# Kernel tuning notes

Hardware: AMD Instinct MI355X
Metric: run time of the kernel (lower is better)

## Reference

```python
import jax, jax.numpy as jnp
import numpy as np

D_EMBED = 1024
HEAD_SIZE = 64
BATCH = 8
SEQ = 2048


def setup_inputs() -> dict:
    key = jax.random.key(0)
    kx, kq, kk, kv = jax.random.split(key, 4)
    x = jax.random.normal(kx, (BATCH, SEQ, D_EMBED), dtype=jnp.float32)
    Wq = jax.random.normal(kq, (D_EMBED, HEAD_SIZE), dtype=jnp.float32) * (1.0 / np.sqrt(D_EMBED))
    Wk = jax.random.normal(kk, (D_EMBED, HEAD_SIZE), dtype=jnp.float32) * (1.0 / np.sqrt(D_EMBED))
    Wv = jax.random.normal(kv, (D_EMBED, HEAD_SIZE), dtype=jnp.float32) * (1.0 / np.sqrt(D_EMBED))
    return {"x": x, "Wq": Wq, "Wk": Wk, "Wv": Wv}


def reference(x, Wq, Wk, Wv):
    # x: [B, S, D]; projections -> [B, S, H]
    Q = jnp.einsum('bsd,dh->bsh', x, Wq)
    K = jnp.einsum('bsd,dh->bsh', x, Wk)
    V = jnp.einsum('bsd,dh->bsh', x, Wv)
    S = x.shape[1]
    scores = jnp.einsum('bqh,bkh->bqk', Q, K)  # [B, S, S]
    causal = jnp.tril(jnp.ones((S, S), dtype=bool))
    # mask before scaling (scaling -inf is still -inf; matches original order)
    scores = jnp.where(causal, scores, -jnp.inf)
    scores = scores / jnp.sqrt(jnp.asarray(K.shape[-1], dtype=scores.dtype))
    attn = jax.nn.softmax(scores, axis=-1)
    # dropout_rate = 0.0 (eval): identity
    return jnp.einsum('bqk,bkh->bqh', attn, V)
```

## Files before the change

### kernel.cpp

```cpp
#include <hip/hip_runtime.h>

typedef _Float16 half8_t __attribute__((ext_vector_type(8)));
typedef _Float16 half4_t __attribute__((ext_vector_type(4)));
typedef _Float16 half2_t __attribute__((ext_vector_type(2)));
typedef __fp16 fp16x2 __attribute__((ext_vector_type(2)));
typedef float f32x4 __attribute__((ext_vector_type(4)));

static constexpr int SEQ = 2048;
static constexpr int DEMB = 1024;


__device__ __forceinline__ float fexp2(float x) {
#if __has_builtin(__builtin_amdgcn_exp2f)
  return __builtin_amdgcn_exp2f(x);
#else
  return exp2f(x);
#endif
}

__device__ __forceinline__ half8_t cvt8(float4 a, float4 b) {
  half8_t xf;
  xf[0] = (_Float16)a.x; xf[1] = (_Float16)a.y;
  xf[2] = (_Float16)a.z; xf[3] = (_Float16)a.w;
  xf[4] = (_Float16)b.x; xf[5] = (_Float16)b.y;
  xf[6] = (_Float16)b.z; xf[7] = (_Float16)b.w;
  return xf;
}

__global__ __launch_bounds__(256) void wt_kernel(const float* __restrict__ Wq,
                                                 const float* __restrict__ Wk,
                                                 const float* __restrict__ Wv,
                                                 _Float16* __restrict__ Wt) {
  int i = blockIdx.x * 256 + threadIdx.x;
  int n = i >> 10;
  int k = i & 1023;
  const float* W = (n < 64) ? Wq : ((n < 128) ? Wk : Wv);
  Wt[i] = (_Float16)W[k * 64 + (n & 63)];
}

__global__ __launch_bounds__(256) void proj_kernel(const float* __restrict__ x,
                                                   const _Float16* __restrict__ Wt,
                                                   _Float16* __restrict__ Qh,
                                                   _Float16* __restrict__ Kh,
                                                   _Float16* __restrict__ Vt) {
  __shared__ __align__(16) char sbuf[8192];

  const int tid = threadIdx.x;
  const int lane = tid & 63;
  const int wv = tid >> 6;
  const int g = lane >> 4;
  const int c = lane & 15;
  const int m0 = blockIdx.x * 32;

  const int srow = tid >> 3;
  const float* xsrc = x + (size_t)(m0 + srow) * DEMB + (tid & 7) * 4;
  char* lws = sbuf + ((unsigned)(tid * 16) ^ (unsigned)((srow & 7) << 4));

  const unsigned sw = (unsigned)((c & 7) << 4);
  const unsigned rA = (unsigned)(c * 128 + g * 32);

  const f32x4 zero = {0.f, 0.f, 0.f, 0.f};
  f32x4 acc[2][3];
#pragma unroll
  for (int ms = 0; ms < 2; ++ms)
#pragma unroll
    for (int j = 0; j < 3; ++j) acc[ms][j] = zero;

  const _Float16* wb0 = Wt + (size_t)((3 * wv + 0) * 16 + c) * 1024 + 8 * g;
  const _Float16* wb1 = Wt + (size_t)((3 * wv + 1) * 16 + c) * 1024 + 8 * g;
  const _Float16* wb2 = Wt + (size_t)((3 * wv + 2) * 16 + c) * 1024 + 8 * g;
  half8_t wf0 = *(const half8_t*)(wb0);
  half8_t wf1 = *(const half8_t*)(wb1);
  half8_t wf2 = *(const half8_t*)(wb2);

  {
    float4 xa = *(const float4*)(xsrc);
    *(float4*)(lws) = xa;
  }
  __syncthreads();

  for (int t = 0; t < 31; ++t) {
    const int kc = (t + 1) * 32;
    float4 xn = *(const float4*)(xsrc + kc);
    half8_t wn0 = *(const half8_t*)(wb0 + kc);
    half8_t wn1 = *(const half8_t*)(wb1 + kc);
    half8_t wn2 = *(const half8_t*)(wb2 + kc);
    const char* rb = sbuf + (t & 1) * 4096;
    half8_t xf[2];
#pragma unroll
    for (int ms = 0; ms < 2; ++ms) {
      const unsigned base = rA + (unsigned)(ms * 2048);
      float4 xlo = *(const float4*)(rb + (base ^ sw));
      float4 xhi = *(const float4*)(rb + ((base + 16) ^ sw));
      xf[ms] = cvt8(xlo, xhi);
    }
#pragma unroll
    for (int j = 0; j < 3; ++j) {
      half8_t wcur = (j == 0) ? wf0 : ((j == 1) ? wf1 : wf2);
      const int nt = 3 * wv + j;
      if (nt < 8) {
        acc[0][j] = __builtin_amdgcn_mfma_f32_16x16x32_f16(wcur, xf[0], acc[0][j], 0, 0, 0);
        acc[1][j] = __builtin_amdgcn_mfma_f32_16x16x32_f16(wcur, xf[1], acc[1][j], 0, 0, 0);
      } else {
        acc[0][j] = __builtin_amdgcn_mfma_f32_16x16x32_f16(xf[0], wcur, acc[0][j], 0, 0, 0);
        acc[1][j] = __builtin_amdgcn_mfma_f32_16x16x32_f16(xf[1], wcur, acc[1][j], 0, 0, 0);
      }
    }
    wf0 = wn0; wf1 = wn1; wf2 = wn2;
    *(float4*)(lws + ((t + 1) & 1) * 4096) = xn;
    __syncthreads();
  }
  {
    const char* rb = sbuf + 4096;
    half8_t xf[2];
#pragma unroll
    for (int ms = 0; ms < 2; ++ms) {
      const unsigned base = rA + (unsigned)(ms * 2048);
      float4 xlo = *(const float4*)(rb + (base ^ sw));
      float4 xhi = *(const float4*)(rb + ((base + 16) ^ sw));
      xf[ms] = cvt8(xlo, xhi);
    }
#pragma unroll
    for (int j = 0; j < 3; ++j) {
      half8_t wcur = (j == 0) ? wf0 : ((j == 1) ? wf1 : wf2);
      const int nt = 3 * wv + j;
      if (nt < 8) {
        acc[0][j] = __builtin_amdgcn_mfma_f32_16x16x32_f16(wcur, xf[0], acc[0][j], 0, 0, 0);
        acc[1][j] = __builtin_amdgcn_mfma_f32_16x16x32_f16(wcur, xf[1], acc[1][j], 0, 0, 0);
      } else {
        acc[0][j] = __builtin_amdgcn_mfma_f32_16x16x32_f16(xf[0], wcur, acc[0][j], 0, 0, 0);
        acc[1][j] = __builtin_amdgcn_mfma_f32_16x16x32_f16(xf[1], wcur, acc[1][j], 0, 0, 0);
      }
    }
  }

  const int b = m0 >> 11;
#pragma unroll
  for (int j = 0; j < 3; ++j) {
    const int nt = 3 * wv + j;
#pragma unroll
    for (int ms = 0; ms < 2; ++ms) {
      half4_t h;
      h[0] = (_Float16)acc[ms][j][0]; h[1] = (_Float16)acc[ms][j][1];
      h[2] = (_Float16)acc[ms][j][2]; h[3] = (_Float16)acc[ms][j][3];
      if (nt < 4) {
        *(half4_t*)(Qh + (size_t)(m0 + ms * 16 + c) * 64 + nt * 16 + 4 * g) = h;
      } else if (nt < 8) {
        *(half4_t*)(Kh + (size_t)(m0 + ms * 16 + c) * 64 + (nt - 4) * 16 + 4 * g) = h;
      } else {
        const int hh = (nt - 8) * 16 + c;
        const int s0 = (m0 & 2047) + ms * 16 + 4 * g;
        *(half4_t*)(Vt + (size_t)(b * 64 + hh) * 2048 + s0) = h;
      }
    }
  }
}

__device__ __forceinline__ void flash_tile(int q0, int wv, int g, int c,
                                           const _Float16* __restrict__ Qb,
                                           const _Float16* __restrict__ Kb,
                                           const _Float16* __restrict__ Vb,
                                           f32x4 (&acc)[4], float& m2, float& lsum) {
  const f32x4 zero = {0.f, 0.f, 0.f, 0.f};
  const float CS = 0.18033688011112042f;
  const int q_lane = q0 + c;
  const int nb = ((q0 + 15) >> 6) + 1;

  const _Float16* Qrow = Qb + (size_t)(q0 + c) * 64;
  half8_t qf0 = *(const half8_t*)(Qrow + 8 * g);
  half8_t qf1 = *(const half8_t*)(Qrow + 32 + 8 * g);

  const int addr_u01 = (2 * (g & 1)) * 64 + c * 4;
  const int addr_u23 = (2 * (g & 1) + 1) * 64 + c * 4;
  const bool glo = (g < 2);

  for (int jb = wv; jb < nb; jb += 8) {
    const int k0 = jb * 64;
    f32x4 sacc[4];
#pragma unroll
    for (int kt = 0; kt < 4; ++kt) {
      const _Float16* Krow = Kb + (size_t)(k0 + kt * 16 + c) * 64;
      half8_t kf0 = *(const half8_t*)(Krow + 8 * g);
      half8_t kf1 = *(const half8_t*)(Krow + 32 + 8 * g);
      f32x4 t = zero;
      t = __builtin_amdgcn_mfma_f32_16x16x32_f16(kf0, qf0, t, 0, 0, 0);
      t = __builtin_amdgcn_mfma_f32_16x16x32_f16(kf1, qf1, t, 0, 0, 0);
      sacc[kt] = t;
    }
    half8_t vf0[4], vf1[4];
#pragma unroll
    for (int ht = 0; ht < 4; ++ht) {
      const _Float16* Vrow = Vb + (size_t)(16 * ht + c) * 2048 + k0;
      vf0[ht] = *(const half8_t*)(Vrow + 8 * g);
      vf1[ht] = *(const half8_t*)(Vrow + 32 + 8 * g);
    }
    const bool full = (k0 + 63 <= q0);
    float pv[16];
    float bmax = -3.0e38f;
#pragma unroll
    for (int kt = 0; kt < 4; ++kt) {
#pragma unroll
      for (int r = 0; r < 4; ++r) {
        float sv = sacc[kt][r] * CS;
        if (!full) {
          int kidx = k0 + kt * 16 + 4 * g + r;
          sv = (kidx > q_lane) ? -3.0e38f : sv;
        }
        pv[kt * 4 + r] = sv;
        bmax = fmaxf(bmax, sv);
      }
    }
    bmax = fmaxf(bmax, __shfl_xor(bmax, 16));
    bmax = fmaxf(bmax, __shfl_xor(bmax, 32));
    const float mnew = fmaxf(m2, bmax);
    const float fsc = fexp2(m2 - mnew);
    m2 = mnew;
    float psum = 0.f;
#pragma unroll
    for (int t = 0; t < 16; ++t) {
      pv[t] = fexp2(pv[t] - m2);
      psum += pv[t];
    }
    lsum = lsum * fsc + psum;
#pragma unroll
    for (int ht = 0; ht < 4; ++ht) {
#pragma unroll
      for (int r = 0; r < 4; ++r) acc[ht][r] *= fsc;
    }
    int h2[8];
#pragma unroll
    for (int kt = 0; kt < 4; ++kt) {
#pragma unroll
      for (int bb = 0; bb < 2; ++bb) {
        fp16x2 hv = __builtin_amdgcn_cvt_pkrtz(pv[kt * 4 + 2 * bb],
                                               pv[kt * 4 + 2 * bb + 1]);
        h2[kt * 2 + bb] = __builtin_bit_cast(int, hv);
      }
    }
    half8_t pf0, pf1;
#pragma unroll
    for (int u = 0; u < 4; ++u) {
      const int addr = (u < 2) ? addr_u01 : addr_u23;
#pragma unroll
      for (int h = 0; h < 2; ++h) {
        int r1 = __builtin_amdgcn_ds_bpermute(addr, h2[4 * h + (u & 1)]);
        int r2 = __builtin_amdgcn_ds_bpermute(addr, h2[4 * h + 2 + (u & 1)]);
        half2_t t = __builtin_bit_cast(half2_t, glo ? r1 : r2);
        if (h == 0) { pf0[2 * u] = t[0]; pf0[2 * u + 1] = t[1]; }
        else        { pf1[2 * u] = t[0]; pf1[2 * u + 1] = t[1]; }
      }
    }
#pragma unroll
    for (int ht = 0; ht < 4; ++ht) {
      acc[ht] = __builtin_amdgcn_mfma_f32_16x16x32_f16(vf0[ht], pf0, acc[ht], 0, 0, 0);
      acc[ht] = __builtin_amdgcn_mfma_f32_16x16x32_f16(vf1[ht], pf1, acc[ht], 0, 0, 0);
    }
  }
}

__device__ __forceinline__ void combine_tile(char* shraw, int tid, int wv, int g, int c,
                                             int b, int q0, f32x4 (&acc)[4],
                                             float m2, float lsum,
                                             float* __restrict__ out) {
  float* Mm = (float*)(shraw + 34816);
  float* Ll = (float*)(shraw + 35328);
  lsum += __shfl_xor(lsum, 16);
  lsum += __shfl_xor(lsum, 32);
  Mm[wv * 16 + c] = m2;
  Ll[wv * 16 + c] = lsum;
  float* OmW = (float*)shraw + wv * 1088 + c * 68;
#pragma unroll
  for (int ht = 0; ht < 4; ++ht) {
    *(f32x4*)(OmW + ht * 16 + 4 * g) = acc[ht];
  }
  __syncthreads();
  const int r = tid & 15;
  const int cp = tid >> 4;
  const float* OmF = (const float*)shraw;
  float mf = Mm[r];
#pragma unroll
  for (int i = 1; i < 8; ++i) mf = fmaxf(mf, Mm[i * 16 + r]);
  float lf = 0.f, o0 = 0.f, o1 = 0.f;
#pragma unroll
  for (int i = 0; i < 8; ++i) {
    float sc = fexp2(Mm[i * 16 + r] - mf);
    lf += Ll[i * 16 + r] * sc;
    const float* p = OmF + i * 1088 + r * 68 + 2 * cp;
    o0 += p[0] * sc;
    o1 += p[1] * sc;
  }
  const float inv = 1.0f / lf;
  float2 o;
  o.x = o0 * inv;
  o.y = o1 * inv;
  *(float2*)(out + (size_t)(b * 2048 + q0 + r) * 64 + 2 * cp) = o;
}

__global__ __launch_bounds__(512) void attn_kernel(const _Float16* __restrict__ Qh,
                                                   const _Float16* __restrict__ Kh,
                                                   const _Float16* __restrict__ Vt,
                                                   float* __restrict__ out) {
  __shared__ __align__(16) char shraw[35840];

  const int tid = threadIdx.x;
  const int lane = tid & 63;
  const int wv = tid >> 6;
  const int g = lane >> 4;
  const int c = lane & 15;
  const int pr = blockIdx.x & 63;
  const int b = blockIdx.x >> 6;
  const int q0A = pr * 16;
  const int q0B = (127 - pr) * 16;

  const _Float16* Qb = Qh + (size_t)b * 2048 * 64;
  const _Float16* Kb = Kh + (size_t)b * 2048 * 64;
  const _Float16* Vb = Vt + (size_t)b * 64 * 2048;

  const f32x4 zero = {0.f, 0.f, 0.f, 0.f};
  f32x4 accA[4], accB[4];
#pragma unroll
  for (int t = 0; t < 4; ++t) { accA[t] = zero; accB[t] = zero; }
  float mA = -3.0e38f, lA = 0.f;
  float mB = -3.0e38f, lB = 0.f;

  flash_tile(q0A, wv, g, c, Qb, Kb, Vb, accA, mA, lA);
  flash_tile(q0B, wv, g, c, Qb, Kb, Vb, accB, mB, lB);

  combine_tile(shraw, tid, wv, g, c, b, q0A, accA, mA, lA, out);
  __syncthreads();
  combine_tile(shraw, tid, wv, g, c, b, q0B, accB, mB, lB, out);
}

extern "C" void kernel_launch(void* const* d_in, const int* in_sizes, int n_in,
                              void* d_out, int out_size, void* d_ws, size_t ws_size,
                              hipStream_t stream) {
  const float* x  = (const float*)d_in[0];
  const float* Wq = (const float*)d_in[1];
  const float* Wk = (const float*)d_in[2];
  const float* Wv = (const float*)d_in[3];
  char* ws = (char*)d_ws;
  _Float16* Wt = (_Float16*)(ws);
  _Float16* Qh = (_Float16*)(ws + 393216);
  _Float16* Kh = (_Float16*)(ws + 2490368);
  _Float16* Vt = (_Float16*)(ws + 4587520);
  float* out = (float*)d_out;

  wt_kernel<<<dim3(768), dim3(256), 0, stream>>>(Wq, Wk, Wv, Wt);
  proj_kernel<<<dim3(512), dim3(256), 0, stream>>>(x, Wt, Qh, Kh, Vt);
  attn_kernel<<<dim3(512), dim3(512), 0, stream>>>(Qh, Kh, Vt, out);
}
```

Baseline: 70.82 us.

## Stage full x row tile in LDS as fp16 upfront, drop per-step barriers

The projection kernel now loads the block's whole 32x1024 slice of x at the start, with 16 float4 loads in flight per thread. It converts the slice to fp16 and stores it in a 64KB swizzled LDS buffer, behind a single barrier. The main K loop is then fully unrolled and reads fp16 fragments straight from LDS, with no per-iteration global loads of x or __syncthreads. This removes repeated barriers and fp32->fp16 conversions inside the loop and exposes more memory-level parallelism. In exchange, the 64KB of LDS per block lowers occupancy, and the loads can no longer overlap with MFMA work.

```diff
diff --git a/kernel.cpp b/kernel.cpp
--- a/kernel.cpp
+++ b/kernel.cpp
@@ -43,7 +43,7 @@
                                                    _Float16* __restrict__ Qh,
                                                    _Float16* __restrict__ Kh,
                                                    _Float16* __restrict__ Vt) {
-  __shared__ __align__(16) char sbuf[8192];
+  __shared__ __align__(16) char sbuf[65536];
 
   const int tid = threadIdx.x;
   const int lane = tid & 63;
@@ -53,11 +53,31 @@
   const int m0 = blockIdx.x * 32;
 
   const int srow = tid >> 3;
-  const float* xsrc = x + (size_t)(m0 + srow) * DEMB + (tid & 7) * 4;
-  char* lws = sbuf + ((unsigned)(tid * 16) ^ (unsigned)((srow & 7) << 4));
-
-  const unsigned sw = (unsigned)((c & 7) << 4);
-  const unsigned rA = (unsigned)(c * 128 + g * 32);
+  const int p = tid & 7;
+  const float* xsrc = x + (size_t)(m0 + srow) * DEMB + p * 4;
+  const unsigned wbase = (unsigned)(srow * 2048 + p * 8);
+  const unsigned wswz = (unsigned)((srow & 7) << 4);
+
+#pragma unroll
+  for (int q = 0; q < 2; ++q) {
+    float4 v[16];
+#pragma unroll
+    for (int i = 0; i < 16; ++i)
+      v[i] = *(const float4*)(xsrc + (q * 16 + i) * 32);
+#pragma unroll
+    for (int i = 0; i < 16; ++i) {
+      half4_t h;
+      h[0] = (_Float16)v[i].x; h[1] = (_Float16)v[i].y;
+      h[2] = (_Float16)v[i].z; h[3] = (_Float16)v[i].w;
+      const unsigned a = (wbase + (unsigned)((q * 16 + i) * 64)) ^ wswz;
+      *(half4_t*)(sbuf + a) = h;
+    }
+  }
+  __syncthreads();
+
+  const unsigned rsw = (unsigned)((c & 7) << 4);
+  const unsigned rbase0 = (unsigned)(c * 2048 + g * 16);
+  const unsigned rbase1 = (unsigned)((16 + c) * 2048 + g * 16);
 
   const f32x4 zero = {0.f, 0.f, 0.f, 0.f};
   f32x4 acc[2][3];
@@ -73,65 +93,31 @@
   half8_t wf1 = *(const half8_t*)(wb1);
   half8_t wf2 = *(const half8_t*)(wb2);
 
-  {
-    float4 xa = *(const float4*)(xsrc);
-    *(float4*)(lws) = xa;
-  }
-  __syncthreads();
-
-  for (int t = 0; t < 31; ++t) {
-    const int kc = (t + 1) * 32;
-    float4 xn = *(const float4*)(xsrc + kc);
-    half8_t wn0 = *(const half8_t*)(wb0 + kc);
-    half8_t wn1 = *(const half8_t*)(wb1 + kc);
-    half8_t wn2 = *(const half8_t*)(wb2 + kc);
-    const char* rb = sbuf + (t & 1) * 4096;
-    half8_t xf[2];
-#pragma unroll
-    for (int ms = 0; ms < 2; ++ms) {
-      const unsigned base = rA + (unsigned)(ms * 2048);
-      float4 xlo = *(const float4*)(rb + (base ^ sw));
-      float4 xhi = *(const float4*)(rb + ((base + 16) ^ sw));
-      xf[ms] = cvt8(xlo, xhi);
-    }
+#pragma unroll
+  for (int t = 0; t < 32; ++t) {
+    half8_t wn0{}, wn1{}, wn2{};
+    if (t < 31) {
+      const int kc = (t + 1) * 32;
+      wn0 = *(const half8_t*)(wb0 + kc);
+      wn1 = *(const half8_t*)(wb1 + kc);
+      wn2 = *(const half8_t*)(wb2 + kc);
+    }
+    const unsigned co = (unsigned)(t * 64);
+    half8_t xf0 = *(const half8_t*)(sbuf + ((rbase0 + co) ^ rsw));
+    half8_t xf1 = *(const half8_t*)(sbuf + ((rbase1 + co) ^ rsw));
 #pragma unroll
     for (int j = 0; j < 3; ++j) {
       half8_t wcur = (j == 0) ? wf0 : ((j == 1) ? wf1 : wf2);
       const int nt = 3 * wv + j;
       if (nt < 8) {
-        acc[0][j] = __builtin_amdgcn_mfma_f32_16x16x32_f16(wcur, xf[0], acc[0][j], 0, 0, 0);
-        acc[1][j] = __builtin_amdgcn_mfma_f32_16x16x32_f16(wcur, xf[1], acc[1][j], 0, 0, 0);
+        acc[0][j] = __builtin_amdgcn_mfma_f32_16x16x32_f16(wcur, xf0, acc[0][j], 0, 0, 0);
+        acc[1][j] = __builtin_amdgcn_mfma_f32_16x16x32_f16(wcur, xf1, acc[1][j], 0, 0, 0);
       } else {
-        acc[0][j] = __builtin_amdgcn_mfma_f32_16x16x32_f16(xf[0], wcur, acc[0][j], 0, 0, 0);
-        acc[1][j] = __builtin_amdgcn_mfma_f32_16x16x32_f16(xf[1], wcur, acc[1][j], 0, 0, 0);
+        acc[0][j] = __builtin_amdgcn_mfma_f32_16x16x32_f16(xf0, wcur, acc[0][j], 0, 0, 0);
+        acc[1][j] = __builtin_amdgcn_mfma_f32_16x16x32_f16(xf1, wcur, acc[1][j], 0, 0, 0);
       }
     }
     wf0 = wn0; wf1 = wn1; wf2 = wn2;
-    *(float4*)(lws + ((t + 1) & 1) * 4096) = xn;
-    __syncthreads();
-  }
-  {
-    const char* rb = sbuf + 4096;
-    half8_t xf[2];
-#pragma unroll
-    for (int ms = 0; ms < 2; ++ms) {
-      const unsigned base = rA + (unsigned)(ms * 2048);
-      float4 xlo = *(const float4*)(rb + (base ^ sw));
-      float4 xhi = *(const float4*)(rb + ((base + 16) ^ sw));
-      xf[ms] = cvt8(xlo, xhi);
-    }
-#pragma unroll
-    for (int j = 0; j < 3; ++j) {
-      half8_t wcur = (j == 0) ? wf0 : ((j == 1) ? wf1 : wf2);
-      const int nt = 3 * wv + j;
-      if (nt < 8) {
-        acc[0][j] = __builtin_amdgcn_mfma_f32_16x16x32_f16(wcur, xf[0], acc[0][j], 0, 0, 0);
-        acc[1][j] = __builtin_amdgcn_mfma_f32_16x16x32_f16(wcur, xf[1], acc[1][j], 0, 0, 0);
-      } else {
-        acc[0][j] = __builtin_amdgcn_mfma_f32_16x16x32_f16(xf[0], wcur, acc[0][j], 0, 0, 0);
-        acc[1][j] = __builtin_amdgcn_mfma_f32_16x16x32_f16(xf[1], wcur, acc[1][j], 0, 0, 0);
-      }
-    }
   }
 
   const int b = m0 >> 11;
```

New measurement: 79.96 us. 12.9% more time.

## Split projection GEMM along K into four partial passes plus reduce kernel

Applied to the files above, without the earlier changes.

The projection kernel is split into four K-slices per 32-row tile, raising the block count from 512 to 2048. Each block writes fp32 partial accumulators to a workspace buffer. A separate reduce kernel sums the four partials, converts to half, and scatters into the Q, K and V^T layouts. This aims to increase parallelism across CUs, at the cost of substantial extra global memory traffic for the partials and an additional kernel launch.

```diff
diff --git a/kernel.cpp b/kernel.cpp
--- a/kernel.cpp
+++ b/kernel.cpp
@@ -38,11 +38,9 @@
   Wt[i] = (_Float16)W[k * 64 + (n & 63)];
 }
 
-__global__ __launch_bounds__(256) void proj_kernel(const float* __restrict__ x,
-                                                   const _Float16* __restrict__ Wt,
-                                                   _Float16* __restrict__ Qh,
-                                                   _Float16* __restrict__ Kh,
-                                                   _Float16* __restrict__ Vt) {
+__global__ __launch_bounds__(256) void proj_split_kernel(const float* __restrict__ x,
+                                                         const _Float16* __restrict__ Wt,
+                                                         float* __restrict__ P) {
   __shared__ __align__(16) char sbuf[8192];
 
   const int tid = threadIdx.x;
@@ -50,10 +48,13 @@
   const int wv = tid >> 6;
   const int g = lane >> 4;
   const int c = lane & 15;
-  const int m0 = blockIdx.x * 32;
+  const int mt = blockIdx.x >> 2;
+  const int kq = blockIdx.x & 3;
+  const int m0 = mt * 32;
+  const int k0 = kq * 256;
 
   const int srow = tid >> 3;
-  const float* xsrc = x + (size_t)(m0 + srow) * DEMB + (tid & 7) * 4;
+  const float* xsrc = x + (size_t)(m0 + srow) * DEMB + k0 + (tid & 7) * 4;
   char* lws = sbuf + ((unsigned)(tid * 16) ^ (unsigned)((srow & 7) << 4));
 
   const unsigned sw = (unsigned)((c & 7) << 4);
@@ -66,9 +67,9 @@
 #pragma unroll
     for (int j = 0; j < 3; ++j) acc[ms][j] = zero;
 
-  const _Float16* wb0 = Wt + (size_t)((3 * wv + 0) * 16 + c) * 1024 + 8 * g;
-  const _Float16* wb1 = Wt + (size_t)((3 * wv + 1) * 16 + c) * 1024 + 8 * g;
-  const _Float16* wb2 = Wt + (size_t)((3 * wv + 2) * 16 + c) * 1024 + 8 * g;
+  const _Float16* wb0 = Wt + (size_t)((3 * wv + 0) * 16 + c) * 1024 + k0 + 8 * g;
+  const _Float16* wb1 = Wt + (size_t)((3 * wv + 1) * 16 + c) * 1024 + k0 + 8 * g;
+  const _Float16* wb2 = Wt + (size_t)((3 * wv + 2) * 16 + c) * 1024 + k0 + 8 * g;
   half8_t wf0 = *(const half8_t*)(wb0);
   half8_t wf1 = *(const half8_t*)(wb1);
   half8_t wf2 = *(const half8_t*)(wb2);
@@ -79,7 +80,7 @@
   }
   __syncthreads();
 
-  for (int t = 0; t < 31; ++t) {
+  for (int t = 0; t < 7; ++t) {
     const int kc = (t + 1) * 32;
     float4 xn = *(const float4*)(xsrc + kc);
     half8_t wn0 = *(const half8_t*)(wb0 + kc);
@@ -134,25 +135,56 @@
     }
   }
 
-  const int b = m0 >> 11;
+  const size_t S = 3145728;
+  float* Pp = P + (size_t)kq * S;
 #pragma unroll
   for (int j = 0; j < 3; ++j) {
-    const int nt = 3 * wv + j;
 #pragma unroll
     for (int ms = 0; ms < 2; ++ms) {
-      half4_t h;
-      h[0] = (_Float16)acc[ms][j][0]; h[1] = (_Float16)acc[ms][j][1];
-      h[2] = (_Float16)acc[ms][j][2]; h[3] = (_Float16)acc[ms][j][3];
-      if (nt < 4) {
-        *(half4_t*)(Qh + (size_t)(m0 + ms * 16 + c) * 64 + nt * 16 + 4 * g) = h;
-      } else if (nt < 8) {
-        *(half4_t*)(Kh + (size_t)(m0 + ms * 16 + c) * 64 + (nt - 4) * 16 + 4 * g) = h;
-      } else {
-        const int hh = (nt - 8) * 16 + c;
-        const int s0 = (m0 & 2047) + ms * 16 + 4 * g;
-        *(half4_t*)(Vt + (size_t)(b * 64 + hh) * 2048 + s0) = h;
-      }
-    }
+      const size_t u = ((size_t)(mt * 4 + wv) * 6 + (size_t)(j * 2 + ms)) * 64 + lane;
+      *(f32x4*)(Pp + u * 4) = acc[ms][j];
+    }
+  }
+}
+
+__global__ __launch_bounds__(256) void reduce_kernel(const float* __restrict__ P,
+                                                     _Float16* __restrict__ Qh,
+                                                     _Float16* __restrict__ Kh,
+                                                     _Float16* __restrict__ Vt) {
+  const size_t S = 3145728;
+  const int u = blockIdx.x * 256 + threadIdx.x;
+  const int lane = u & 63;
+  const int v = u >> 6;
+  const int jm = v % 6;
+  const int t6 = v / 6;
+  const int wv = t6 & 3;
+  const int mt = t6 >> 2;
+  const int j = jm >> 1;
+  const int ms = jm & 1;
+  const int g = lane >> 4;
+  const int c = lane & 15;
+  const int m0 = mt * 32;
+
+  f32x4 s0 = *(const f32x4*)(P + (size_t)u * 4);
+  f32x4 s1 = *(const f32x4*)(P + S + (size_t)u * 4);
+  f32x4 s2 = *(const f32x4*)(P + 2 * S + (size_t)u * 4);
+  f32x4 s3 = *(const f32x4*)(P + 3 * S + (size_t)u * 4);
+  f32x4 sum = (s0 + s1) + (s2 + s3);
+
+  half4_t h;
+  h[0] = (_Float16)sum[0]; h[1] = (_Float16)sum[1];
+  h[2] = (_Float16)sum[2]; h[3] = (_Float16)sum[3];
+
+  const int nt = 3 * wv + j;
+  if (nt < 4) {
+    *(half4_t*)(Qh + (size_t)(m0 + ms * 16 + c) * 64 + nt * 16 + 4 * g) = h;
+  } else if (nt < 8) {
+    *(half4_t*)(Kh + (size_t)(m0 + ms * 16 + c) * 64 + (nt - 4) * 16 + 4 * g) = h;
+  } else {
+    const int b = m0 >> 11;
+    const int hh = (nt - 8) * 16 + c;
+    const int ss = (m0 & 2047) + ms * 16 + 4 * g;
+    *(half4_t*)(Vt + (size_t)(b * 64 + hh) * 2048 + ss) = h;
   }
 }
 
@@ -343,9 +375,11 @@
   _Float16* Qh = (_Float16*)(ws + 393216);
   _Float16* Kh = (_Float16*)(ws + 2490368);
   _Float16* Vt = (_Float16*)(ws + 4587520);
+  float* P = (float*)(ws + 6684672);
   float* out = (float*)d_out;
 
   wt_kernel<<<dim3(768), dim3(256), 0, stream>>>(Wq, Wk, Wv, Wt);
-  proj_kernel<<<dim3(512), dim3(256), 0, stream>>>(x, Wt, Qh, Kh, Vt);
+  proj_split_kernel<<<dim3(2048), dim3(256), 0, stream>>>(x, Wt, P);
+  reduce_kernel<<<dim3(3072), dim3(256), 0, stream>>>(P, Qh, Kh, Vt);
   attn_kernel<<<dim3(512), dim3(512), 0, stream>>>(Qh, Kh, Vt, out);
 }
```

After: 84.39 us. 19.2% more time.
